# Kernel tuning notes

Hardware: AMD Instinct MI355X
Metric: run time of the kernel (lower is better)

Reference implementation:

```python
import jax, jax.numpy as jnp
import numpy as np

NEG_SLOPE = 0.2  # DGL GATConv default leaky_relu slope


def gat_conv(x, src, dst, W, attn_l, attn_r, bias, res_W):
    """DGL GATConv (eval mode, residual=True with linear res_fc, bias).
    x: [N, F_in]; src/dst: [E]; W: [F_in, H*D]; attn_l/r: [H, D];
    bias: [H*D]; res_W: [F_in, H*D]. Returns [N, H, D]."""
    N = x.shape[0]
    H, D = attn_l.shape
    feat = (x @ W).reshape(N, H, D)
    el = jnp.sum(feat * attn_l, axis=-1)  # [N, H]
    er = jnp.sum(feat * attn_r, axis=-1)  # [N, H]
    e = jax.nn.leaky_relu(el[src] + er[dst], NEG_SLOPE)  # [E, H]
    # edge softmax over incoming edges of each dst node (numerically stable)
    m = jnp.full((N, H), -jnp.inf, dtype=e.dtype).at[dst].max(e)
    ex = jnp.exp(e - m[dst])
    s = jnp.zeros((N, H), dtype=e.dtype).at[dst].add(ex)
    alpha = ex / s[dst]  # [E, H]
    # scatter-aggregate messages alpha * feat[src] into dst
    rst = jnp.zeros((N, H, D), dtype=x.dtype).at[dst].add(alpha[:, :, None] * feat[src])
    rst = rst + (x @ res_W).reshape(N, H, D) + bias.reshape(1, H, D)
    return rst


def setup_inputs() -> dict:
    key = jax.random.key(0)
    N, E, F_IN, HID, OUT, H = 20000, 320000, 128, 128, 128, 4
    ks = jax.random.split(key, 32)
    ki = iter(range(32))

    def rn(shape, scale=0.05):
        return jax.random.normal(ks[next(ki)], shape, dtype=jnp.float32) * scale

    inp = {
        "n_feat": jax.random.normal(ks[next(ki)], (N, F_IN), dtype=jnp.float32),
        "src": jax.random.randint(ks[next(ki)], (E,), 0, N, dtype=jnp.int32),
        "dst": jax.random.randint(ks[next(ki)], (E,), 0, N, dtype=jnp.int32),
        # input GATConv: F_IN -> H x HID
        "W0": rn((F_IN, H * HID)), "al0": rn((H, HID)), "ar0": rn((H, HID)),
        "b0": rn((H * HID,)), "rW0": rn((F_IN, H * HID)),
        "DW0": rn((H * HID, HID)), "Db0": rn((HID,)),
        # middle GATConv: HID -> H x HID
        "W1": rn((HID, H * HID)), "al1": rn((H, HID)), "ar1": rn((H, HID)),
        "b1": rn((H * HID,)), "rW1": rn((HID, H * HID)),
        "DW1": rn((H * HID, HID)), "Db1": rn((HID,)),
        # output GATConv: HID -> H x OUT
        "W2": rn((HID, H * OUT)), "al2": rn((H, OUT)), "ar2": rn((H, OUT)),
        "b2": rn((H * OUT,)), "rW2": rn((HID, H * OUT)),
    }
    return inp


def reference(n_feat, src, dst,
              W0, al0, ar0, b0, rW0, DW0, Db0,
              W1, al1, ar1, b1, rW1, DW1, Db1,
              W2, al2, ar2, b2, rW2):
    N = n_feat.shape[0]
    relu = jax.nn.relu
    # input GAT block
    h = relu(gat_conv(n_feat, src, dst, W0, al0, ar0, b0, rW0))  # [N, H, HID]
    h = relu(h.reshape(N, -1) @ DW0 + Db0)                        # [N, HID]
    # middle GAT block
    h = relu(gat_conv(h, src, dst, W1, al1, ar1, b1, rW1))
    h = relu(h.reshape(N, -1) @ DW1 + Db1)
    # output GAT + head-mean + graph max pooling (single graph)
    h = relu(gat_conv(h, src, dst, W2, al2, ar2, b2, rW2))        # [N, H, OUT]
    h = relu(jnp.mean(h, axis=-2))                                 # [N, OUT]
    return jnp.max(h, axis=0, keepdims=True)                       # [1, OUT]
```

## Files before the change

kernel.cpp:

```cpp
#include <hip/hip_runtime.h>
#include <hip/hip_bf16.h>


typedef __attribute__((ext_vector_type(8))) short bf16x8;
typedef __attribute__((ext_vector_type(4))) float f32x4;
typedef __hip_bfloat16 bf16_t;

#define NEG_SLOPE 0.2f

__device__ __forceinline__ unsigned int pack_bf16(float lo, float hi) {
  return (((unsigned int)__bfloat16_as_ushort(__float2bfloat16(hi))) << 16) |
         (unsigned int)__bfloat16_as_ushort(__float2bfloat16(lo));
}

__device__ __forceinline__ float leaky_exp(float e) {
  e = (e > 0.f) ? e : NEG_SLOPE * e;
  return __expf(e);
}

__device__ __forceinline__ void gload_lds16(const void* g, void* l) {
  __builtin_amdgcn_global_load_lds(
      (const __attribute__((address_space(1))) void*)g,
      (__attribute__((address_space(3))) void*)l, 16, 0, 0);
}

__global__ __launch_bounds__(256) void mega_prep(
    const float* __restrict__ W0, const float* __restrict__ rW0,
    const float* __restrict__ W1, const float* __restrict__ rW1,
    const float* __restrict__ W2, const float* __restrict__ rW2,
    const float* __restrict__ DW0, const float* __restrict__ DW1,
    const float* __restrict__ al0, const float* __restrict__ ar0,
    const float* __restrict__ al1, const float* __restrict__ ar1,
    const float* __restrict__ al2, const float* __restrict__ ar2,
    const float* __restrict__ n_feat, bf16_t* __restrict__ wts,
    float* __restrict__ ALR, bf16_t* __restrict__ xbf,
    int* __restrict__ counts, float* __restrict__ partials, int N) {
  __shared__ float tile[32][33];
  int b = blockIdx.x, tid = threadIdx.x;
  int r = tid >> 5, c = tid & 31;

  if (b < 384) {
    int mat = b >> 6;
    int t = b & 63;
    int kt = t >> 4, nt = t & 15;
    int L = mat >> 1, isR = mat & 1;
    const float* S = (L == 0) ? (isR ? rW0 : W0)
                   : (L == 1) ? (isR ? rW1 : W1) : (isR ? rW2 : W2);
    bf16_t* D = wts + L * 131072 + isR * 65536;
#pragma unroll
    for (int rr = 0; rr < 4; rr++)
      tile[r + rr * 8][c] = S[(kt * 32 + r + rr * 8) * 512 + nt * 32 + c];
    __syncthreads();
#pragma unroll
    for (int rr = 0; rr < 4; rr++)
      D[(nt * 32 + r + rr * 8) * 128 + kt * 32 + c] =
          __float2bfloat16(tile[c][r + rr * 8]);
  } else if (b < 512) {
    int i = b - 384;
    int mat = i >> 6;
    int t = i & 63;
    int kt = t & 15, nt = t >> 4;
    const float* S = mat ? DW1 : DW0;
    bf16_t* D = wts + 393216 + mat * 65536;
#pragma unroll
    for (int rr = 0; rr < 4; rr++)
      tile[r + rr * 8][c] = S[(kt * 32 + r + rr * 8) * 128 + nt * 32 + c];
    __syncthreads();
#pragma unroll
    for (int rr = 0; rr < 4; rr++)
      D[(nt * 32 + r + rr * 8) * 512 + kt * 32 + c] =
          __float2bfloat16(tile[c][r + rr * 8]);
  } else if (b < 524) {
    int idx = (b - 512) * 256 + tid;
    if (idx < 3072) {
      int L = idx >> 10;
      int k = (idx >> 3) & 127;
      int cc = idx & 7;
      int h = cc & 3;
      const float* W = (L == 0) ? W0 : (L == 1) ? W1 : W2;
      const float* a = (cc < 4) ? ((L == 0) ? al0 : (L == 1) ? al1 : al2)
                                : ((L == 0) ? ar0 : (L == 1) ? ar1 : ar2);
      float s = 0.f;
      for (int d = 0; d < 128; d++) s += W[k * 512 + h * 128 + d] * a[h * 128 + d];
      ALR[idx] = s;
    }
  } else if (b < 3024) {
    int i = ((b - 524) * 256 + tid) * 4;
    if (i < N * 128) {
      float4 v = *(const float4*)(n_feat + i);
      xbf[i + 0] = __float2bfloat16(v.x);
      xbf[i + 1] = __float2bfloat16(v.y);
      xbf[i + 2] = __float2bfloat16(v.z);
      xbf[i + 3] = __float2bfloat16(v.w);
    }
  } else {
    for (int i = tid; i < N; i += 256) counts[i] = 0;
    for (int i = tid; i < 64 * 128; i += 256) partials[i] = 0.f;
  }
}

template <bool COUNT>
__global__ __launch_bounds__(256) void gemm128el(
    const bf16_t* __restrict__ A, const bf16_t* __restrict__ Bt,
    const float* __restrict__ ALRl, bf16_t* __restrict__ featB,
    bf16_t* __restrict__ resB,
    float* __restrict__ el, float* __restrict__ er, int M, int K,
    const int* __restrict__ dst, int* __restrict__ counts, int E) {
  __shared__ bf16_t As[128 * 64];
  __shared__ bf16_t Bs[128 * 64];
  int tid = threadIdx.x;
  int rowBase = blockIdx.y * 128;

  if (COUNT && blockIdx.x == 9) {
    int stride = gridDim.y * 256;
    for (int i = blockIdx.y * 256 + tid; i < E; i += stride)
      atomicAdd(&counts[dst[i]], 1);
    return;
  }

  if (blockIdx.x == 8) {
    float* sALR = (float*)As;
#pragma unroll
    for (int j = 0; j < 4; j++) sALR[tid * 4 + j] = ALRl[tid * 4 + j];
    __syncthreads();
    int row = rowBase + (tid >> 1);
    int half = tid & 1;
    if (row < M) {
      const bf16_t* xr = A + (size_t)row * K + half * 64;
      float s[8] = {};
#pragma unroll
      for (int g = 0; g < 8; g++) {
        bf16x8 v = *(const bf16x8*)(xr + g * 8);
#pragma unroll
        for (int e = 0; e < 8; e++) {
          float f = __uint_as_float(((unsigned int)(unsigned short)v[e]) << 16);
          const float* Ak = sALR + (half * 64 + g * 8 + e) * 8;
#pragma unroll
          for (int cc = 0; cc < 8; cc++) s[cc] += f * Ak[cc];
        }
      }
#pragma unroll
      for (int cc = 0; cc < 8; cc++) s[cc] += __shfl_xor(s[cc], 1);
      if (half == 0)
        *(float4*)(el + row * 4) = make_float4(s[0], s[1], s[2], s[3]);
      else
        *(float4*)(er + row * 4) = make_float4(s[4], s[5], s[6], s[7]);
    }
    return;
  }

  int lane = tid & 63, wave = tid >> 6;
  int q = lane >> 4, r16 = lane & 15;
  int wm = (wave >> 1) * 64, wn = (wave & 1) * 64;
  int colBase = blockIdx.x * 128;
  bf16_t* Cb = (colBase < 512) ? featB : resB;
  int colOff = (colBase < 512) ? colBase : colBase - 512;

  f32x4 acc[4][4] = {};

  for (int k0 = 0; k0 < K; k0 += 64) {
#pragma unroll
    for (int p = 0; p < 4; p++) {
      int slotb = (wave * 4 + p) * 64;
      int s = slotb + lane;
      int r = s >> 3;
      int c = (s & 7) ^ (r & 7);
      int gr = rowBase + r;
      if (gr > M - 1) gr = M - 1;
      gload_lds16(A + (size_t)gr * K + k0 + c * 8, (char*)As + (size_t)slotb * 16);
      gload_lds16(Bt + (size_t)(colBase + r) * K + k0 + c * 8,
                  (char*)Bs + (size_t)slotb * 16);
    }
    __syncthreads();
#pragma unroll
    for (int ks = 0; ks < 64; ks += 32) {
      int koff = ks >> 3;
      bf16x8 af[4], bfr[4];
#pragma unroll
      for (int i = 0; i < 4; i++) {
        int R = wm + i * 16 + r16;
        int slot = R * 8 + ((q + koff) ^ (R & 7));
        af[i] = *(const bf16x8*)((const char*)As + (size_t)slot * 16);
      }
#pragma unroll
      for (int j = 0; j < 4; j++) {
        int R = wn + j * 16 + r16;
        int slot = R * 8 + ((q + koff) ^ (R & 7));
        bfr[j] = *(const bf16x8*)((const char*)Bs + (size_t)slot * 16);
      }
#pragma unroll
      for (int i = 0; i < 4; i++)
#pragma unroll
        for (int j = 0; j < 4; j++)
          acc[i][j] = __builtin_amdgcn_mfma_f32_16x16x32_bf16(af[i], bfr[j], acc[i][j], 0, 0, 0);
    }
    __syncthreads();
  }

  int odd = lane & 1;
  int colb0 = r16 & ~1;
#pragma unroll
  for (int i = 0; i < 4; i++) {
#pragma unroll
    for (int r = 0; r < 4; r++) {
      int row = rowBase + wm + i * 16 + q * 4 + r;
#pragma unroll
      for (int jp = 0; jp < 2; jp++) {
        float a0 = acc[i][2 * jp][r];
        float a1 = acc[i][2 * jp + 1][r];
        float p0 = __shfl_xor(a0, 1);
        float p1 = __shfl_xor(a1, 1);
        float lo = odd ? p1 : a0;
        float hi = odd ? a1 : p0;
        int col = colOff + wn + (2 * jp + odd) * 16 + colb0;
        if (row < M)
          *(unsigned int*)(Cb + (size_t)row * 512 + col) = pack_bf16(lo, hi);
      }
    }
  }
}

__global__ __launch_bounds__(256) void mfma_gemm64(
    const bf16_t* __restrict__ A, const bf16_t* __restrict__ Bt,
    const float* __restrict__ bias, bf16_t* __restrict__ C,
    int M, int ldc, int K) {
  __shared__ bf16_t As[64 * 64];
  __shared__ bf16_t Bs[64 * 64];
  int tid = threadIdx.x;
  int lane = tid & 63, wave = tid >> 6;
  int q = lane >> 4, r16 = lane & 15;
  int wm = (wave >> 1) * 32, wn = (wave & 1) * 32;
  int rowBase = blockIdx.y * 64, colBase = blockIdx.x * 64;

  f32x4 acc[2][2] = {};

  for (int k0 = 0; k0 < K; k0 += 64) {
#pragma unroll
    for (int p = 0; p < 2; p++) {
      int slotb = (wave * 2 + p) * 64;
      int s = slotb + lane;
      int r = s >> 3;
      int c = (s & 7) ^ (r & 7);
      int gr = rowBase + r;
      if (gr > M - 1) gr = M - 1;
      gload_lds16(A + (size_t)gr * K + k0 + c * 8, (char*)As + (size_t)slotb * 16);
      gload_lds16(Bt + (size_t)(colBase + r) * K + k0 + c * 8,
                  (char*)Bs + (size_t)slotb * 16);
    }
    __syncthreads();
#pragma unroll
    for (int ks = 0; ks < 64; ks += 32) {
      int koff = ks >> 3;
      bf16x8 af[2], bfr[2];
#pragma unroll
      for (int i = 0; i < 2; i++) {
        int R = wm + i * 16 + r16;
        int slot = R * 8 + ((q + koff) ^ (R & 7));
        af[i] = *(const bf16x8*)((const char*)As + (size_t)slot * 16);
      }
#pragma unroll
      for (int j = 0; j < 2; j++) {
        int R = wn + j * 16 + r16;
        int slot = R * 8 + ((q + koff) ^ (R & 7));
        bfr[j] = *(const bf16x8*)((const char*)Bs + (size_t)slot * 16);
      }
#pragma unroll
      for (int i = 0; i < 2; i++)
#pragma unroll
        for (int j = 0; j < 2; j++)
          acc[i][j] = __builtin_amdgcn_mfma_f32_16x16x32_bf16(af[i], bfr[j], acc[i][j], 0, 0, 0);
    }
    __syncthreads();
  }

  int odd = lane & 1;
  int colb0 = r16 & ~1;
#pragma unroll
  for (int i = 0; i < 2; i++) {
#pragma unroll
    for (int r = 0; r < 4; r++) {
      int row = rowBase + wm + i * 16 + q * 4 + r;
      float a0 = acc[i][0][r];
      float a1 = acc[i][1][r];
      float p0 = __shfl_xor(a0, 1);
      float p1 = __shfl_xor(a1, 1);
      float lo = odd ? p1 : a0;
      float hi = odd ? a1 : p0;
      int col = colBase + wn + odd * 16 + colb0;
      if (row < M) {
        float o0 = fmaxf(lo + bias[col], 0.f);
        float o1 = fmaxf(hi + bias[col + 1], 0.f);
        *(unsigned int*)(C + (size_t)row * ldc + col) = pack_bf16(o0, o1);
      }
    }
  }
}

__global__ __launch_bounds__(1024) void scan_kernel(const int* __restrict__ counts,
                                                    int* __restrict__ row_ptr,
                                                    int* __restrict__ cursor, int N) {
  __shared__ int sums[1024];
  int t = threadIdx.x;
  int chunk = (N + 1023) / 1024;
  int begin = t * chunk;
  int end = begin + chunk;
  if (end > N) end = N;
  int s = 0;
  for (int i = begin; i < end; i++) s += counts[i];
  sums[t] = s;
  __syncthreads();
  for (int off = 1; off < 1024; off <<= 1) {
    int v = (t >= off) ? sums[t - off] : 0;
    __syncthreads();
    sums[t] += v;
    __syncthreads();
  }
  int run = (t == 0) ? 0 : sums[t - 1];
  for (int i = begin; i < end; i++) {
    row_ptr[i] = run;
    cursor[i] = run;
    run += counts[i];
  }
  if (t == 1023) row_ptr[N] = sums[1023];
}

__global__ __launch_bounds__(256) void scatter_w_kernel(
    const int* __restrict__ src, const int* __restrict__ dst,
    int* __restrict__ cursor, int* __restrict__ edge_src,
    int* __restrict__ edge_dst, const float* __restrict__ el,
    const float* __restrict__ er, float* __restrict__ wcsr, int E) {
  int i = blockIdx.x * blockDim.x + threadIdx.x;
  if (i < E) {
    int s = src[i];
    int d = dst[i];
    int pos = atomicAdd(&cursor[d], 1);
    edge_src[pos] = s;
    edge_dst[pos] = d;
    float4 elv = *(const float4*)(el + s * 4);
    float4 erv = *(const float4*)(er + d * 4);
    float4 w;
    w.x = leaky_exp(elv.x + erv.x);
    w.y = leaky_exp(elv.y + erv.y);
    w.z = leaky_exp(elv.z + erv.z);
    w.w = leaky_exp(elv.w + erv.w);
    *(float4*)(wcsr + (size_t)pos * 4) = w;
  }
}

__global__ __launch_bounds__(256) void w_pass_kernel(
    const int* __restrict__ edge_src, const int* __restrict__ edge_dst,
    const float* __restrict__ el, const float* __restrict__ er,
    float* __restrict__ wcsr, int E) {
  int p = blockIdx.x * blockDim.x + threadIdx.x;
  if (p < E) {
    int s = edge_src[p];
    int d = edge_dst[p];
    float4 elv = *(const float4*)(el + s * 4);
    float4 erv = *(const float4*)(er + d * 4);
    float4 w;
    w.x = leaky_exp(elv.x + erv.x);
    w.y = leaky_exp(elv.y + erv.y);
    w.z = leaky_exp(elv.z + erv.z);
    w.w = leaky_exp(elv.w + erv.w);
    *(float4*)(wcsr + (size_t)p * 4) = w;
  }
}

template <bool POOL>
__global__ __launch_bounds__(256) void gat_agg_kernel(
    const bf16_t* __restrict__ featB,
    const bf16_t* __restrict__ resB,
    const float* __restrict__ wcsr,
    const float* __restrict__ bias, const int* __restrict__ row_ptr,
    const int* __restrict__ edge_src, bf16_t* __restrict__ out,
    float* __restrict__ partials, int N) {
  __shared__ float accL[4][64][8];
  __shared__ float ssumL[4][4];
  int n = blockIdx.x;
  int tid = threadIdx.x;
  int wave = tid >> 6, lane = tid & 63;
  int hh = lane >> 4;
  int start = row_ptr[n];
  int deg = row_ptr[n + 1] - start;

  float acc[8] = {};
  float ssum = 0.f;
  const bf16_t* fbase = featB + (size_t)lane * 8;
  for (int i = wave; i < deg; i += 4) {
    int p = start + i;
    int s = edge_src[p];
    float wv = wcsr[(size_t)p * 4 + hh];
    ssum += wv;
    uint4 f = *(const uint4*)(fbase + (size_t)s * 512);
    unsigned int u[4] = {f.x, f.y, f.z, f.w};
#pragma unroll
    for (int j = 0; j < 4; j++) {
      acc[2 * j] += wv * __uint_as_float(u[j] << 16);
      acc[2 * j + 1] += wv * __uint_as_float(u[j] & 0xffff0000u);
    }
  }
  *(float4*)&accL[wave][lane][0] = make_float4(acc[0], acc[1], acc[2], acc[3]);
  *(float4*)&accL[wave][lane][4] = make_float4(acc[4], acc[5], acc[6], acc[7]);
  if ((lane & 15) == 0) ssumL[wave][hh] = ssum;
  __syncthreads();

  int d = tid * 2;
  int l = d >> 3, j = d & 7;
  float a0 = 0.f, a1 = 0.f;
#pragma unroll
  for (int w = 0; w < 4; w++) {
    a0 += accL[w][l][j];
    a1 += accL[w][l][j + 1];
  }
  int h = tid >> 6;
  float ssum4 = ssumL[0][h] + ssumL[1][h] + ssumL[2][h] + ssumL[3][h];
  float inv = (deg > 0) ? 1.f / ssum4 : 0.f;
  unsigned int ru = *(const unsigned int*)(resB + (size_t)n * 512 + d);
  float2 bv = *(const float2*)(bias + d);
  float o0 = fmaxf(a0 * inv + __uint_as_float(ru << 16) + bv.x, 0.f);
  float o1 = fmaxf(a1 * inv + __uint_as_float(ru & 0xffff0000u) + bv.y, 0.f);

  if (!POOL) {
    *(unsigned int*)(out + (size_t)n * 512 + d) = pack_bf16(o0, o1);
  } else {
    float2* red = (float2*)accL;
    __syncthreads();
    red[tid] = make_float2(o0, o1);
    __syncthreads();
    if (tid < 64) {
      float m0 = 0.25f * (red[tid].x + red[tid + 64].x + red[tid + 128].x + red[tid + 192].x);
      float m1 = 0.25f * (red[tid].y + red[tid + 64].y + red[tid + 128].y + red[tid + 192].y);
      float* slot = partials + (n & 63) * 128;
      atomicMax((int*)slot + 2 * tid, __float_as_int(m0));
      atomicMax((int*)slot + 2 * tid + 1, __float_as_int(m1));
    }
  }
}

__global__ __launch_bounds__(128) void pool_finish(const float* __restrict__ partials,
                                                   float* __restrict__ out) {
  int d = threadIdx.x;
  float m = 0.f;
#pragma unroll 8
  for (int s = 0; s < 64; s++) m = fmaxf(m, partials[s * 128 + d]);
  out[d] = m;
}

extern "C" void kernel_launch(void* const* d_in, const int* in_sizes, int n_in,
                              void* d_out, int out_size, void* d_ws, size_t ws_size,
                              hipStream_t stream) {
  const float* n_feat = (const float*)d_in[0];
  const int* src = (const int*)d_in[1];
  const int* dst = (const int*)d_in[2];
  const float* W0 = (const float*)d_in[3];
  const float* al0 = (const float*)d_in[4];
  const float* ar0 = (const float*)d_in[5];
  const float* b0 = (const float*)d_in[6];
  const float* rW0 = (const float*)d_in[7];
  const float* DW0 = (const float*)d_in[8];
  const float* Db0 = (const float*)d_in[9];
  const float* W1 = (const float*)d_in[10];
  const float* al1 = (const float*)d_in[11];
  const float* ar1 = (const float*)d_in[12];
  const float* b1 = (const float*)d_in[13];
  const float* rW1 = (const float*)d_in[14];
  const float* DW1 = (const float*)d_in[15];
  const float* Db1 = (const float*)d_in[16];
  const float* W2 = (const float*)d_in[17];
  const float* al2 = (const float*)d_in[18];
  const float* ar2 = (const float*)d_in[19];
  const float* b2 = (const float*)d_in[20];
  const float* rW2 = (const float*)d_in[21];

  const int N = in_sizes[0] / 128;
  const int E = in_sizes[1];

  bf16_t* xbf = (bf16_t*)d_ws;
  bf16_t* featB = xbf + (size_t)N * 128;
  bf16_t* resB = featB + (size_t)N * 512;
  bf16_t* outC = resB + (size_t)N * 512;
  bf16_t* denseD = outC + (size_t)N * 512;
  bf16_t* wts = denseD + (size_t)N * 128;
  float* ALR = (float*)(wts + 524288);
  float* el = ALR + 3072;
  float* er = el + (size_t)N * 4;
  float* partials = er + (size_t)N * 4;
  float* wcsr = partials + 64 * 128;
  int* counts = (int*)(wcsr + (size_t)E * 4);
  int* row_ptr = counts + N;
  int* cursor = row_ptr + (N + 1);
  int* edge_src = cursor + N;
  int* edge_dst = edge_src + E;

  bf16_t* FW0 = wts;
  bf16_t* FW1 = wts + 131072;
  bf16_t* FW2 = wts + 262144;
  bf16_t* DWt0 = wts + 393216;
  bf16_t* DWt1 = wts + 458752;

  mega_prep<<<3025, 256, 0, stream>>>(
      W0, rW0, W1, rW1, W2, rW2, DW0, DW1,
      al0, ar0, al1, ar1, al2, ar2,
      n_feat, wts, ALR, xbf, counts, partials, N);

  int nRow = (N + 127) / 128;
  dim3 gF0(10, nRow);
  dim3 gF(9, nRow);
  dim3 gD(2, (N + 63) / 64);
  int gE = (E + 255) / 256;

  gemm128el<true><<<gF0, 256, 0, stream>>>(xbf, FW0, ALR, featB, resB, el, er,
                                           N, 128, dst, counts, E);
  scan_kernel<<<1, 1024, 0, stream>>>(counts, row_ptr, cursor, N);
  scatter_w_kernel<<<gE, 256, 0, stream>>>(src, dst, cursor, edge_src, edge_dst,
                                           el, er, wcsr, E);

  gat_agg_kernel<false><<<N, 256, 0, stream>>>(featB, resB, wcsr, b0, row_ptr,
                                               edge_src, outC, nullptr, N);
  mfma_gemm64<<<gD, 256, 0, stream>>>(outC, DWt0, Db0, denseD, N, 128, 512);
  gemm128el<false><<<gF, 256, 0, stream>>>(denseD, FW1, ALR + 1024, featB, resB,
                                           el, er, N, 128, nullptr, nullptr, 0);
  w_pass_kernel<<<gE, 256, 0, stream>>>(edge_src, edge_dst, el, er, wcsr, E);
  gat_agg_kernel<false><<<N, 256, 0, stream>>>(featB, resB, wcsr, b1, row_ptr,
                                               edge_src, outC, nullptr, N);
  mfma_gemm64<<<gD, 256, 0, stream>>>(outC, DWt1, Db1, denseD, N, 128, 512);
  gemm128el<false><<<gF, 256, 0, stream>>>(denseD, FW2, ALR + 2048, featB, resB,
                                           el, er, N, 128, nullptr, nullptr, 0);
  w_pass_kernel<<<gE, 256, 0, stream>>>(edge_src, edge_dst, el, er, wcsr, E);
  gat_agg_kernel<true><<<N, 256, 0, stream>>>(featB, resB, wcsr, b2, row_ptr,
                                              edge_src, nullptr, partials, N);
  pool_finish<<<1, 128, 0, stream>>>(partials, (float*)d_out);
}
```

Measured before the change: 424.1 us.

## Slice GAT aggregation by feature column, transpose edge weights, separate pooling pass

Replaces the one-block-per-node aggregation with blocks that each handle 8 nodes times a 64-column slice, with the slice index in the low bits of the block index so the 8 slices of a node group run on adjacent blocks. Edge weights are stored head-major (transposed) so each slice reads a contiguous per-head weight array. The goal is better L2 locality for gathered source features and more work per block. Final pooling moves out of the aggregation into a separate kernel that reads the bf16 output and does atomic max directly into the zero-initialised output. The cost is an extra write and read of the last layer's output, plus duplicated edge_src and weight reads across the 8 slices.

```diff
diff --git a/kernel.cpp b/kernel.cpp
--- a/kernel.cpp
+++ b/kernel.cpp
@@ -34,7 +34,7 @@
     const float* __restrict__ al2, const float* __restrict__ ar2,
     const float* __restrict__ n_feat, bf16_t* __restrict__ wts,
     float* __restrict__ ALR, bf16_t* __restrict__ xbf,
-    int* __restrict__ counts, float* __restrict__ partials, int N) {
+    int* __restrict__ counts, float* __restrict__ d_out_f, int N) {
   __shared__ float tile[32][33];
   int b = blockIdx.x, tid = threadIdx.x;
   int r = tid >> 5, c = tid & 31;
@@ -95,7 +95,7 @@
     }
   } else {
     for (int i = tid; i < N; i += 256) counts[i] = 0;
-    for (int i = tid; i < 64 * 128; i += 256) partials[i] = 0.f;
+    if (tid < 128) d_out_f[tid] = 0.f;
   }
 }
 
@@ -328,7 +328,7 @@
     const int* __restrict__ src, const int* __restrict__ dst,
     int* __restrict__ cursor, int* __restrict__ edge_src,
     int* __restrict__ edge_dst, const float* __restrict__ el,
-    const float* __restrict__ er, float* __restrict__ wcsr, int E) {
+    const float* __restrict__ er, float* __restrict__ wcsrT, int E) {
   int i = blockIdx.x * blockDim.x + threadIdx.x;
   if (i < E) {
     int s = src[i];
@@ -338,112 +338,102 @@
     edge_dst[pos] = d;
     float4 elv = *(const float4*)(el + s * 4);
     float4 erv = *(const float4*)(er + d * 4);
-    float4 w;
-    w.x = leaky_exp(elv.x + erv.x);
-    w.y = leaky_exp(elv.y + erv.y);
-    w.z = leaky_exp(elv.z + erv.z);
-    w.w = leaky_exp(elv.w + erv.w);
-    *(float4*)(wcsr + (size_t)pos * 4) = w;
+    wcsrT[0 * E + pos] = leaky_exp(elv.x + erv.x);
+    wcsrT[1 * E + pos] = leaky_exp(elv.y + erv.y);
+    wcsrT[2 * E + pos] = leaky_exp(elv.z + erv.z);
+    wcsrT[3 * E + pos] = leaky_exp(elv.w + erv.w);
   }
 }
 
 __global__ __launch_bounds__(256) void w_pass_kernel(
     const int* __restrict__ edge_src, const int* __restrict__ edge_dst,
     const float* __restrict__ el, const float* __restrict__ er,
-    float* __restrict__ wcsr, int E) {
+    float* __restrict__ wcsrT, int E) {
   int p = blockIdx.x * blockDim.x + threadIdx.x;
   if (p < E) {
     int s = edge_src[p];
     int d = edge_dst[p];
     float4 elv = *(const float4*)(el + s * 4);
     float4 erv = *(const float4*)(er + d * 4);
-    float4 w;
-    w.x = leaky_exp(elv.x + erv.x);
-    w.y = leaky_exp(elv.y + erv.y);
-    w.z = leaky_exp(elv.z + erv.z);
-    w.w = leaky_exp(elv.w + erv.w);
-    *(float4*)(wcsr + (size_t)p * 4) = w;
-  }
-}
-
-template <bool POOL>
-__global__ __launch_bounds__(256) void gat_agg_kernel(
+    wcsrT[0 * E + p] = leaky_exp(elv.x + erv.x);
+    wcsrT[1 * E + p] = leaky_exp(elv.y + erv.y);
+    wcsrT[2 * E + p] = leaky_exp(elv.z + erv.z);
+    wcsrT[3 * E + p] = leaky_exp(elv.w + erv.w);
+  }
+}
+
+__global__ __launch_bounds__(256) void gat_agg_sliced(
     const bf16_t* __restrict__ featB,
     const bf16_t* __restrict__ resB,
-    const float* __restrict__ wcsr,
+    const float* __restrict__ wcsrT,
     const float* __restrict__ bias, const int* __restrict__ row_ptr,
-    const int* __restrict__ edge_src, bf16_t* __restrict__ out,
-    float* __restrict__ partials, int N) {
-  __shared__ float accL[4][64][8];
-  __shared__ float ssumL[4][4];
-  int n = blockIdx.x;
+    const int* __restrict__ edge_src, bf16_t* __restrict__ out, int N, int E) {
+  __shared__ float accS[4][8][64];
+  __shared__ float ssumS[4][8];
+  int bx = blockIdx.x;
+  int s = bx & 7;
+  int chunk = bx >> 3;
   int tid = threadIdx.x;
-  int wave = tid >> 6, lane = tid & 63;
-  int hh = lane >> 4;
-  int start = row_ptr[n];
-  int deg = row_ptr[n + 1] - start;
+  int gid = tid >> 3, t8 = tid & 7;
+  int nslot = gid & 7, sub = gid >> 3;
+  int n = chunk * 8 + nslot;
+  int head = s >> 1;
 
   float acc[8] = {};
   float ssum = 0.f;
-  const bf16_t* fbase = featB + (size_t)lane * 8;
-  for (int i = wave; i < deg; i += 4) {
-    int p = start + i;
-    int s = edge_src[p];
-    float wv = wcsr[(size_t)p * 4 + hh];
-    ssum += wv;
-    uint4 f = *(const uint4*)(fbase + (size_t)s * 512);
-    unsigned int u[4] = {f.x, f.y, f.z, f.w};
-#pragma unroll
-    for (int j = 0; j < 4; j++) {
-      acc[2 * j] += wv * __uint_as_float(u[j] << 16);
-      acc[2 * j + 1] += wv * __uint_as_float(u[j] & 0xffff0000u);
-    }
-  }
-  *(float4*)&accL[wave][lane][0] = make_float4(acc[0], acc[1], acc[2], acc[3]);
-  *(float4*)&accL[wave][lane][4] = make_float4(acc[4], acc[5], acc[6], acc[7]);
-  if ((lane & 15) == 0) ssumL[wave][hh] = ssum;
+  if (n < N) {
+    int start = row_ptr[n];
+    int deg = row_ptr[n + 1] - start;
+    const float* wbase = wcsrT + (size_t)head * E;
+    const bf16_t* fbase = featB + s * 64 + t8 * 8;
+    for (int i = sub; i < deg; i += 4) {
+      int p = start + i;
+      int e = edge_src[p];
+      float wv = wbase[p];
+      ssum += wv;
+      uint4 f = *(const uint4*)(fbase + (size_t)e * 512);
+      unsigned int u[4] = {f.x, f.y, f.z, f.w};
+#pragma unroll
+      for (int j = 0; j < 4; j++) {
+        acc[2 * j] += wv * __uint_as_float(u[j] << 16);
+        acc[2 * j + 1] += wv * __uint_as_float(u[j] & 0xffff0000u);
+      }
+    }
+  }
+  *(float4*)&accS[sub][nslot][t8 * 8] = make_float4(acc[0], acc[1], acc[2], acc[3]);
+  *(float4*)&accS[sub][nslot][t8 * 8 + 4] = make_float4(acc[4], acc[5], acc[6], acc[7]);
+  if (t8 == 0) ssumS[sub][nslot] = ssum;
   __syncthreads();
 
-  int d = tid * 2;
-  int l = d >> 3, j = d & 7;
-  float a0 = 0.f, a1 = 0.f;
-#pragma unroll
-  for (int w = 0; w < 4; w++) {
-    a0 += accL[w][l][j];
-    a1 += accL[w][l][j + 1];
-  }
-  int h = tid >> 6;
-  float ssum4 = ssumL[0][h] + ssumL[1][h] + ssumL[2][h] + ssumL[3][h];
-  float inv = (deg > 0) ? 1.f / ssum4 : 0.f;
-  unsigned int ru = *(const unsigned int*)(resB + (size_t)n * 512 + d);
-  float2 bv = *(const float2*)(bias + d);
+  int idx = tid * 2;
+  int ns2 = idx >> 6;
+  int d2 = idx & 63;
+  int n2 = chunk * 8 + ns2;
+  if (n2 >= N) return;
+  float a0 = accS[0][ns2][d2] + accS[1][ns2][d2] + accS[2][ns2][d2] + accS[3][ns2][d2];
+  float a1 = accS[0][ns2][d2 + 1] + accS[1][ns2][d2 + 1] + accS[2][ns2][d2 + 1] +
+             accS[3][ns2][d2 + 1];
+  float ssum4 = ssumS[0][ns2] + ssumS[1][ns2] + ssumS[2][ns2] + ssumS[3][ns2];
+  float inv = (ssum4 > 0.f) ? 1.f / ssum4 : 0.f;
+  int dg = s * 64 + d2;
+  unsigned int ru = *(const unsigned int*)(resB + (size_t)n2 * 512 + dg);
+  float2 bv = *(const float2*)(bias + dg);
   float o0 = fmaxf(a0 * inv + __uint_as_float(ru << 16) + bv.x, 0.f);
   float o1 = fmaxf(a1 * inv + __uint_as_float(ru & 0xffff0000u) + bv.y, 0.f);
-
-  if (!POOL) {
-    *(unsigned int*)(out + (size_t)n * 512 + d) = pack_bf16(o0, o1);
-  } else {
-    float2* red = (float2*)accL;
-    __syncthreads();
-    red[tid] = make_float2(o0, o1);
-    __syncthreads();
-    if (tid < 64) {
-      float m0 = 0.25f * (red[tid].x + red[tid + 64].x + red[tid + 128].x + red[tid + 192].x);
-      float m1 = 0.25f * (red[tid].y + red[tid + 64].y + red[tid + 128].y + red[tid + 192].y);
-      float* slot = partials + (n & 63) * 128;
-      atomicMax((int*)slot + 2 * tid, __float_as_int(m0));
-      atomicMax((int*)slot + 2 * tid + 1, __float_as_int(m1));
-    }
-  }
-}
-
-__global__ __launch_bounds__(128) void pool_finish(const float* __restrict__ partials,
-                                                   float* __restrict__ out) {
+  *(unsigned int*)(out + (size_t)n2 * 512 + dg) = pack_bf16(o0, o1);
+}
+
+__global__ __launch_bounds__(128) void pool_kernel(const bf16_t* __restrict__ g,
+                                                   float* __restrict__ out, int N) {
   int d = threadIdx.x;
-  float m = 0.f;
-#pragma unroll 8
-  for (int s = 0; s < 64; s++) m = fmaxf(m, partials[s * 128 + d]);
-  out[d] = m;
+  float mx = 0.f;
+  for (int n = blockIdx.x; n < N; n += gridDim.x) {
+    const bf16_t* p = g + (size_t)n * 512 + d;
+    float v = 0.25f * (__bfloat162float(p[0]) + __bfloat162float(p[128]) +
+                       __bfloat162float(p[256]) + __bfloat162float(p[384]));
+    mx = fmaxf(mx, v);
+  }
+  atomicMax((int*)out + d, __float_as_int(mx));
 }
 
 extern "C" void kernel_launch(void* const* d_in, const int* in_sizes, int n_in,
@@ -484,9 +474,8 @@
   float* ALR = (float*)(wts + 524288);
   float* el = ALR + 3072;
   float* er = el + (size_t)N * 4;
-  float* partials = er + (size_t)N * 4;
-  float* wcsr = partials + 64 * 128;
-  int* counts = (int*)(wcsr + (size_t)E * 4);
+  float* wcsrT = er + (size_t)N * 4;
+  int* counts = (int*)(wcsrT + (size_t)E * 4);
   int* row_ptr = counts + N;
   int* cursor = row_ptr + (N + 1);
   int* edge_src = cursor + N;
@@ -501,33 +490,34 @@
   mega_prep<<<3025, 256, 0, stream>>>(
       W0, rW0, W1, rW1, W2, rW2, DW0, DW1,
       al0, ar0, al1, ar1, al2, ar2,
-      n_feat, wts, ALR, xbf, counts, partials, N);
+      n_feat, wts, ALR, xbf, counts, (float*)d_out, N);
 
   int nRow = (N + 127) / 128;
   dim3 gF0(10, nRow);
   dim3 gF(9, nRow);
   dim3 gD(2, (N + 63) / 64);
   int gE = (E + 255) / 256;
+  int gAgg = ((N + 7) / 8) * 8;
 
   gemm128el<true><<<gF0, 256, 0, stream>>>(xbf, FW0, ALR, featB, resB, el, er,
                                            N, 128, dst, counts, E);
   scan_kernel<<<1, 1024, 0, stream>>>(counts, row_ptr, cursor, N);
   scatter_w_kernel<<<gE, 256, 0, stream>>>(src, dst, cursor, edge_src, edge_dst,
-                                           el, er, wcsr, E);
-
-  gat_agg_kernel<false><<<N, 256, 0, stream>>>(featB, resB, wcsr, b0, row_ptr,
-                                               edge_src, outC, nullptr, N);
+                                           el, er, wcsrT, E);
+
+  gat_agg_sliced<<<gAgg, 256, 0, stream>>>(featB, resB, wcsrT, b0, row_ptr,
+                                           edge_src, outC, N, E);
   mfma_gemm64<<<gD, 256, 0, stream>>>(outC, DWt0, Db0, denseD, N, 128, 512);
   gemm128el<false><<<gF, 256, 0, stream>>>(denseD, FW1, ALR + 1024, featB, resB,
                                            el, er, N, 128, nullptr, nullptr, 0);
-  w_pass_kernel<<<gE, 256, 0, stream>>>(edge_src, edge_dst, el, er, wcsr, E);
-  gat_agg_kernel<false><<<N, 256, 0, stream>>>(featB, resB, wcsr, b1, row_ptr,
-                                               edge_src, outC, nullptr, N);
+  w_pass_kernel<<<gE, 256, 0, stream>>>(edge_src, edge_dst, el, er, wcsrT, E);
+  gat_agg_sliced<<<gAgg, 256, 0, stream>>>(featB, resB, wcsrT, b1, row_ptr,
+                                           edge_src, outC, N, E);
   mfma_gemm64<<<gD, 256, 0, stream>>>(outC, DWt1, Db1, denseD, N, 128, 512);
   gemm128el<false><<<gF, 256, 0, stream>>>(denseD, FW2, ALR + 2048, featB, resB,
                                            el, er, N, 128, nullptr, nullptr, 0);
-  w_pass_kernel<<<gE, 256, 0, stream>>>(edge_src, edge_dst, el, er, wcsr, E);
-  gat_agg_kernel<true><<<N, 256, 0, stream>>>(featB, resB, wcsr, b2, row_ptr,
-                                              edge_src, nullptr, partials, N);
-  pool_finish<<<1, 128, 0, stream>>>(partials, (float*)d_out);
-}
+  w_pass_kernel<<<gE, 256, 0, stream>>>(edge_src, edge_dst, el, er, wcsrT, E);
+  gat_agg_sliced<<<gAgg, 256, 0, stream>>>(featB, resB, wcsrT, b2, row_ptr,
+                                           edge_src, outC, N, E);
+  pool_kernel<<<256, 128, 0, stream>>>(outC, (float*)d_out, N);
+}
```

After: 446.4 us. 1.05x slower.
